# Optimization experiments

Measured on AMD Instinct MI355X. Metric: run time of the kernel, lower is better.

Reference implementation:

```python
import jax, jax.numpy as jnp
import numpy as np

N, F, OUT = 8192, 256, 256


def setup_inputs() -> dict:
    key = jax.random.key(0)
    ks = jax.random.split(key, 8)
    s = 1.0 / np.sqrt(F)
    return {
        "features": jax.random.normal(ks[0], (N, F), jnp.float32),
        "key_features": jax.random.normal(ks[1], (N, F), jnp.float32),
        "adj_matrix": jax.random.uniform(ks[2], (N, N), jnp.float32),
        "W_d": jax.random.normal(ks[3], (2 * F, F), jnp.float32) * (1.0 / np.sqrt(2 * F)),
        "b_d": jnp.zeros((F,), jnp.float32),
        "W_o": jax.random.normal(ks[4], (F, OUT), jnp.float32) * s,
        "b_o": jnp.zeros((OUT,), jnp.float32),
        "W_a": jax.random.normal(ks[5], (F, F), jnp.float32) * s,
        "b_a": jnp.zeros((F,), jnp.float32),
        "W_ao": jax.random.normal(ks[6], (F, OUT), jnp.float32) * s,
        "b_ao": jnp.zeros((OUT,), jnp.float32),
    }


def reference(features, key_features, adj_matrix, W_d, b_d, W_o, b_o, W_a, b_a, W_ao, b_ao):
    n = features.shape[0]
    # masked softmax over rows; self-loop (diagonal) masked out
    neg = jnp.asarray(-1e9, adj_matrix.dtype)
    logits = adj_matrix * 5.0 + jnp.eye(n, dtype=adj_matrix.dtype) * neg
    a = jax.nn.softmax(logits, axis=-1)  # [N, N]
    # sum_j a_ij * concat(x_i, x_j) == concat(x_i * rowsum_i, (A @ X)_i)
    rowsum = jnp.sum(a, axis=-1, keepdims=True)  # == 1, kept for faithfulness
    agg = a @ features  # [N, F]
    neigh = jnp.concatenate([features * rowsum, agg], axis=-1)  # [N, 2F]
    neigh_distill = neigh @ W_d + b_d
    feature_updated = jnp.tanh((features - neigh_distill) @ W_o + b_o)
    # aggregate branch (withAgg=True)
    key_agg = (a @ key_features) @ W_a + b_a
    feature_aggregate = jnp.tanh((key_features + key_agg) @ W_ao + b_ao)
    return (feature_updated, feature_aggregate)
```

## Files before the change

### kernel.cpp

```cpp
#include <hip/hip_runtime.h>
#include <stdint.h>
#include <math.h>


typedef __attribute__((ext_vector_type(4)))  short bf16x4_t;
typedef __attribute__((ext_vector_type(8)))  short bf16x8_t;
typedef __attribute__((ext_vector_type(4)))  float f32x4_t;
typedef __attribute__((ext_vector_type(16))) float f32x16_t;

#define MFMA32(A, B, C) __builtin_amdgcn_mfma_f32_32x32x16_bf16(A, B, C, 0, 0, 0)
#define MFMA16(A, B, C) __builtin_amdgcn_mfma_f32_16x16x32_bf16(A, B, C, 0, 0, 0)

__device__ __forceinline__ unsigned short f2bf(float x) {
    union { float f; unsigned u; } c; c.f = x;
    unsigned u = c.u;
    return (unsigned short)((u + 0x7fffu + ((u >> 16) & 1u)) >> 16);
}
__device__ __forceinline__ unsigned pack2bf(float a, float b) {
    return (unsigned)f2bf(a) | ((unsigned)f2bf(b) << 16);
}
__device__ __forceinline__ float bflo(unsigned u) {
    union { unsigned u; float f; } c; c.u = u << 16; return c.f;
}
__device__ __forceinline__ float bfhi(unsigned u) {
    union { unsigned u; float f; } c; c.u = u & 0xffff0000u; return c.f;
}
__device__ __forceinline__ float exp5(float x) {
    return __builtin_amdgcn_exp2f(7.2134752f * x);
}

__device__ __forceinline__ void gll16(const unsigned short* g, unsigned short* l) {
    __builtin_amdgcn_global_load_lds(
        (const __attribute__((address_space(1))) unsigned int*)(g),
        (__attribute__((address_space(3))) unsigned int*)(l), 16, 0, 0);
}

__global__ __launch_bounds__(256) void transpose_blob(
    const float* __restrict__ src, unsigned short* __restrict__ Xtb,
    unsigned* __restrict__ packdst, int c32base)
{
    __shared__ float tile[32][33];
    const int t = threadIdx.x;
    const int x = t & 31, y4 = (t >> 5) * 4;
    const int r0 = blockIdx.x * 32, c0 = blockIdx.y * 32;
#pragma unroll
    for (int i = 0; i < 4; ++i)
        tile[y4 + i][x] = src[(size_t)(r0 + y4 + i) * 256 + c0 + x];
    __syncthreads();
    const int s = t >> 7, lane = (t >> 1) & 63, e0 = (t & 1) * 4;
    const int kl = s * 16 + (lane >> 5) * 8 + e0;
    const int cl = lane & 31;
    unsigned short* blob = Xtb + ((size_t)blockIdx.x * 16 + (c0 >> 5) + c32base) * 1024;
    uint2 v;
    v.x = pack2bf(tile[kl][cl],     tile[kl + 1][cl]);
    v.y = pack2bf(tile[kl + 2][cl], tile[kl + 3][cl]);
    *(uint2*)(blob + t * 4) = v;
    const int prow = t >> 3, pc = t & 7;
    unsigned* pd = packdst + (size_t)(r0 + prow) * 256 + (c0 >> 1) + pc * 2;
    pd[0] = pack2bf(tile[prow][pc * 4 + 0], tile[prow][pc * 4 + 1]);
    pd[1] = pack2bf(tile[prow][pc * 4 + 2], tile[prow][pc * 4 + 3]);
}

__global__ __launch_bounds__(256) void compose1(
    const float* __restrict__ W_d, const float* __restrict__ W_o,
    const float* __restrict__ b_d, const float* __restrict__ b_o,
    unsigned short* __restrict__ W1t, float* __restrict__ c1)
{
    __shared__ float wrow[256];
    const int k = blockIdx.x, t = threadIdx.x;
    const float* srcrow = (k < 512) ? (W_d + (size_t)k * 256) : b_d;
    wrow[t] = srcrow[t];
    __syncthreads();
    float acc = 0.f;
#pragma unroll 8
    for (int m = 0; m < 256; ++m) acc = fmaf(wrow[m], W_o[(size_t)m * 256 + t], acc);
    if (k < 512)
        W1t[(size_t)t * 512 + k] = f2bf((k < 256 ? W_o[(size_t)k * 256 + t] : 0.f) - acc);
    else
        c1[t] = b_o[t] - acc;
}

__global__ __launch_bounds__(256) void compose2(
    const float* __restrict__ W_a, const float* __restrict__ W_ao,
    const float* __restrict__ b_a, const float* __restrict__ b_ao,
    unsigned short* __restrict__ W2t, float* __restrict__ c2)
{
    __shared__ float wrow[256];
    const int k = blockIdx.x, t = threadIdx.x;
    if (k < 256) {
        W2t[(size_t)t * 512 + k] = f2bf(W_ao[(size_t)k * 256 + t]);
        return;
    }
    const float* srcrow = (k < 512) ? (W_a + (size_t)(k - 256) * 256) : b_a;
    wrow[t] = srcrow[t];
    __syncthreads();
    float acc = 0.f;
#pragma unroll 8
    for (int m = 0; m < 256; ++m) acc = fmaf(wrow[m], W_ao[(size_t)m * 256 + t], acc);
    if (k < 512) W2t[(size_t)t * 512 + k] = f2bf(acc);
    else         c2[t] = b_ao[t] + acc;
}

#define ROWS 32
#define KSLICE 2048
#define NPH 32
#define ASTRIDE 36

struct QA { float4 v[2]; };

__global__ __launch_bounds__(256, 2) void exp_gemm(
    const float* __restrict__ adj, const unsigned short* __restrict__ Xtb,
    unsigned* __restrict__ UpartB, float* __restrict__ sSp)
{
    __shared__ unsigned short sA[2][2][ROWS * ASTRIDE];
    __shared__ unsigned short sB[4][2][4096];

    const int t = threadIdx.x;
    const int w = t >> 6, lane = t & 63, q = lane >> 5, l31 = lane & 31;
    const int xcd = blockIdx.x & 7;
    const int h = xcd >> 1;
    const int rb = ((blockIdx.x >> 3) << 1) | (xcd & 1);
    const int row0 = rb * ROWS;
    const int kbase = h * KSLICE, jbase = h * (KSLICE / 32);

    const int srow = t >> 3, skoff = (t & 7) * 4;
    const int sgrow = row0 + srow;
    const float* adj_row = adj + (size_t)sgrow * 8192 + kbase + skoff;
    const int swoff = srow * ASTRIDE + skoff;

    const unsigned short* XtbW = Xtb + (size_t)jbase * 16384 + (size_t)w * 4096 + lane * 8;
    unsigned short* const sBw = &sB[w][0][0];

    float rs = 0.f;
    f32x16_t acc[4];
#pragma unroll
    for (int ct = 0; ct < 4; ++ct)
#pragma unroll
        for (int e = 0; e < 16; ++e) acc[ct][e] = 0.f;

    QA qa0, qa1, qa2, qa3;

    auto loadAdj = [&](int cidx, QA& qq) {
        qq.v[0] = *(const float4*)(adj_row + (size_t)(cidx * 2 + 0) * 32);
        qq.v[1] = *(const float4*)(adj_row + (size_t)(cidx * 2 + 1) * 32);
    };

    auto stageChunk = [&](int cidx, const QA& qq, int buf) {
#pragma unroll
        for (int ks = 0; ks < 2; ++ks) {
            const float4 v = qq.v[ks];
            float e0 = exp5(v.x);
            float e1 = exp5(v.y);
            float e2 = exp5(v.z);
            float e3 = exp5(v.w);
            const int gk = kbase + (cidx * 2 + ks) * 32 + skoff;
            if (gk + 0 == sgrow) e0 = 0.f;
            if (gk + 1 == sgrow) e1 = 0.f;
            if (gk + 2 == sgrow) e2 = 0.f;
            if (gk + 3 == sgrow) e3 = 0.f;
            rs += (e0 + e1) + (e2 + e3);
            uint2 p; p.x = pack2bf(e0, e1); p.y = pack2bf(e2, e3);
            *(uint2*)(&sA[buf][ks][swoff]) = p;
        }
    };

    auto issueB = [&](int jn, int slot) {
        const unsigned short* src = XtbW + (size_t)jn * 16384;
        unsigned short* dst = sBw + slot * 4096;
#pragma unroll
        for (int k4 = 0; k4 < 8; ++k4)
            gll16(src + k4 * 512, dst + k4 * 512);
    };

    auto consume = [&](int buf, int u, int jnext) {
        const unsigned short* sbp = sBw + u * 4096 + lane * 8;
        bf16x8_t bfr[4][2];
#pragma unroll
        for (int ct = 0; ct < 4; ++ct)
#pragma unroll
            for (int s = 0; s < 2; ++s)
                bfr[ct][s] = *(const bf16x8_t*)(sbp + ct * 1024 + s * 512);
        const unsigned short* sa = &sA[buf][u][0] + l31 * ASTRIDE + q * 8;
        bf16x8_t af[2];
#pragma unroll
        for (int s = 0; s < 2; ++s) {
            const unsigned short* p = sa + s * 16;
            bf16x4_t lo = *(const bf16x4_t*)p;
            bf16x4_t hi = *(const bf16x4_t*)(p + 4);
            af[s] = __builtin_shufflevector(lo, hi, 0, 1, 2, 3, 4, 5, 6, 7);
        }
        asm volatile("s_waitcnt lgkmcnt(0)" ::: "memory");
        issueB(jnext, u);
        __builtin_amdgcn_s_setprio(1);
#pragma unroll
        for (int s = 0; s < 2; ++s)
#pragma unroll
            for (int ct = 0; ct < 4; ++ct)
                acc[ct] = MFMA32(af[s], bfr[ct][s], acc[ct]);
        __builtin_amdgcn_s_setprio(0);
    };

    auto phase = [&](int c, const QA& qstg, QA& qld, int buf) {
        if (c + 1 < NPH) stageChunk(c + 1, qstg, buf ^ 1);
        asm volatile("s_waitcnt vmcnt(10)" ::: "memory");
        consume(buf, 0, (2 * c + 2) & 63);
        asm volatile("s_waitcnt vmcnt(10)" ::: "memory");
        consume(buf, 1, (2 * c + 3) & 63);
        loadAdj((c + 4) & 31, qld);
        asm volatile("s_waitcnt lgkmcnt(0)\n\ts_barrier" ::: "memory");
    };

    issueB(0, 0); issueB(1, 1);
    loadAdj(0, qa0); loadAdj(1, qa1); loadAdj(2, qa2); loadAdj(3, qa3);
    stageChunk(0, qa0, 0);
    asm volatile("s_waitcnt lgkmcnt(0)\n\ts_barrier" ::: "memory");

    for (int c0 = 0; c0 < NPH; c0 += 4) {
        phase(c0 + 0, qa1, qa0, 0);
        phase(c0 + 1, qa2, qa1, 1);
        phase(c0 + 2, qa3, qa2, 0);
        phase(c0 + 3, qa0, qa3, 1);
    }

    rs += __shfl_xor(rs, 1);
    rs += __shfl_xor(rs, 2);
    rs += __shfl_xor(rs, 4);
    if ((t & 7) == 0) sSp[h * 8192 + sgrow] = rs;

    unsigned* upBase = UpartB + (((size_t)h * 256 + rb) * 8 + w * 2) * 1024 + lane;
#pragma unroll
    for (int cp = 0; cp < 2; ++cp)
#pragma unroll
        for (int c2 = 0; c2 < 2; ++c2)
#pragma unroll
            for (int ip = 0; ip < 8; ++ip)
                upBase[(size_t)cp * 1024 + (c2 * 8 + ip) * 64] =
                    pack2bf(acc[cp * 2 + c2][2 * ip], acc[cp * 2 + c2][2 * ip + 1]);
}

__global__ __launch_bounds__(256) void finalize_agg(
    const unsigned* __restrict__ UpartB, const float* __restrict__ sSp,
    unsigned* __restrict__ XcatN, unsigned* __restrict__ Kcat)
{
    __shared__ float sT[32][65];
    __shared__ float sInv[32];

    const int t = threadIdx.x;
    const int rb = blockIdx.x >> 3, wp = blockIdx.x & 7;
    const int row0 = rb * 32;

    if (t < 32) {
        const int r = row0 + t;
        sInv[t] = 1.f / (sSp[r] + sSp[8192 + r] + sSp[16384 + r] + sSp[24576 + r]);
    }

    const int i = t >> 4;
    const int l0 = (t & 15) * 4;
    const int ct2 = i >> 3, ip = i & 7;
    const int qq = l0 >> 5;
    const int rlo = 2 * (ip & 1) + 8 * (ip >> 1) + 4 * qq;
    const int cbase = ct2 * 32 + (l0 & 31);

    float lo[4], hi[4];
#pragma unroll
    for (int j = 0; j < 4; ++j) { lo[j] = 0.f; hi[j] = 0.f; }
#pragma unroll
    for (int h = 0; h < 4; ++h) {
        const unsigned* src = UpartB + (((size_t)h * 256 + rb) * 8 + wp) * 1024
                              + (size_t)i * 64 + l0;
        const uint4 v0 = *(const uint4*)(src);
        const unsigned vv[4] = { v0.x, v0.y, v0.z, v0.w };
#pragma unroll
        for (int j = 0; j < 4; ++j) { lo[j] += bflo(vv[j]); hi[j] += bfhi(vv[j]); }
    }
#pragma unroll
    for (int j = 0; j < 4; ++j) {
        sT[rlo][cbase + j]     = lo[j];
        sT[rlo + 1][cbase + j] = hi[j];
    }
    __syncthreads();

    const int row = t >> 3, cg = (t & 7) * 8;
    const float inv = sInv[row];
    unsigned outv[4];
#pragma unroll
    for (int j = 0; j < 4; ++j)
        outv[j] = pack2bf(sT[row][cg + 2 * j] * inv, sT[row][cg + 2 * j + 1] * inv);
    unsigned* dst = (wp < 4 ? XcatN : Kcat)
                    + (size_t)(row0 + row) * 256 + 128 + (wp & 3) * 32 + (cg >> 1);
    *(uint4*)(dst) = *(const uint4*)(outv);
}

__global__ __launch_bounds__(256) void gemm_out(
    const unsigned short* __restrict__ Aa, const unsigned short* __restrict__ Wta,
    const float* __restrict__ ca,
    const unsigned short* __restrict__ Ab, const unsigned short* __restrict__ Wtb,
    const float* __restrict__ cb,
    float* __restrict__ outa, float* __restrict__ outb)
{
    __shared__ unsigned short sAm[32 * ASTRIDE];
    __shared__ unsigned short sB[256 * ASTRIDE];
    __shared__ float sBias[256];

    const int bid = blockIdx.x;
    const int prob = bid >> 8, tile = bid & 255;
    const unsigned short* A  = prob ? Ab  : Aa;
    const unsigned short* Wt = prob ? Wtb : Wta;
    const float* cvec        = prob ? cb  : ca;
    float* out               = prob ? outb : outa;

    const int t = threadIdx.x, w = t >> 6, lane = t & 63;
    const int m_lo = lane & 15, quad = lane >> 4;
    const int row0 = tile * 32;
    sBias[t] = cvec[t];

    f32x4_t acc[2][4];
#pragma unroll
    for (int a = 0; a < 2; ++a)
#pragma unroll
        for (int b = 0; b < 4; ++b)
#pragma unroll
            for (int e = 0; e < 4; ++e) acc[a][b][e] = 0.f;

    for (int ks = 0; ks < 16; ++ks) {
        const int k0 = ks * 32;
        __syncthreads();
        if (t < 128) {
            bf16x8_t v = *(const bf16x8_t*)(A + (size_t)(row0 + (t >> 2)) * 512 + k0 + (t & 3) * 8);
            unsigned short* d = &sAm[(t >> 2) * ASTRIDE + (t & 3) * 8];
            *(bf16x4_t*)d       = __builtin_shufflevector(v, v, 0, 1, 2, 3);
            *(bf16x4_t*)(d + 4) = __builtin_shufflevector(v, v, 4, 5, 6, 7);
        }
        {
            const unsigned short* src = Wt + (size_t)t * 512 + k0;
            unsigned short* d = &sB[t * ASTRIDE];
#pragma unroll
            for (int j = 0; j < 4; ++j) {
                bf16x8_t v = *(const bf16x8_t*)(src + j * 8);
                *(bf16x4_t*)(d + j * 8)     = __builtin_shufflevector(v, v, 0, 1, 2, 3);
                *(bf16x4_t*)(d + j * 8 + 4) = __builtin_shufflevector(v, v, 4, 5, 6, 7);
            }
        }
        __syncthreads();
        bf16x8_t a0, a1;
        {
            const unsigned short* p = &sAm[m_lo * ASTRIDE + quad * 8];
            bf16x4_t lo = *(const bf16x4_t*)p, hi = *(const bf16x4_t*)(p + 4);
            a0 = __builtin_shufflevector(lo, hi, 0, 1, 2, 3, 4, 5, 6, 7);
            p += 16 * ASTRIDE;
            lo = *(const bf16x4_t*)p; hi = *(const bf16x4_t*)(p + 4);
            a1 = __builtin_shufflevector(lo, hi, 0, 1, 2, 3, 4, 5, 6, 7);
        }
#pragma unroll
        for (int nt = 0; nt < 4; ++nt) {
            const unsigned short* p = &sB[(w * 64 + nt * 16 + m_lo) * ASTRIDE + quad * 8];
            bf16x4_t lo = *(const bf16x4_t*)p, hi = *(const bf16x4_t*)(p + 4);
            bf16x8_t b = __builtin_shufflevector(lo, hi, 0, 1, 2, 3, 4, 5, 6, 7);
            acc[0][nt] = MFMA16(a0, b, acc[0][nt]);
            acc[1][nt] = MFMA16(a1, b, acc[1][nt]);
        }
    }

#pragma unroll
    for (int mt = 0; mt < 2; ++mt)
#pragma unroll
        for (int nt = 0; nt < 4; ++nt) {
            const int col = w * 64 + nt * 16 + m_lo;
#pragma unroll
            for (int r = 0; r < 4; ++r) {
                const int row = row0 + mt * 16 + quad * 4 + r;
                out[(size_t)row * 256 + col] = tanhf(acc[mt][nt][r] + sBias[col]);
            }
        }
}

extern "C" void kernel_launch(void* const* d_in, const int* in_sizes, int n_in,
                              void* d_out, int out_size, void* d_ws, size_t ws_size,
                              hipStream_t stream) {
    const float* features = (const float*)d_in[0];
    const float* key      = (const float*)d_in[1];
    const float* adj      = (const float*)d_in[2];
    const float* W_d  = (const float*)d_in[3];
    const float* b_d  = (const float*)d_in[4];
    const float* W_o  = (const float*)d_in[5];
    const float* b_o  = (const float*)d_in[6];
    const float* W_a  = (const float*)d_in[7];
    const float* b_a  = (const float*)d_in[8];
    const float* W_ao = (const float*)d_in[9];
    const float* b_ao = (const float*)d_in[10];

    float* out1 = (float*)d_out;
    float* out2 = out1 + (size_t)8192 * 256;

    char* ws = (char*)d_ws;
    unsigned short* XcatN = (unsigned short*)(ws);
    unsigned short* Kcat  = (unsigned short*)(ws +  8388608);
    unsigned short* Xtb   = (unsigned short*)(ws + 16777216);
    unsigned*       UpartB= (unsigned*)      (ws + 25165824);
    float*          sSp   = (float*)         (ws + 58720256);
    unsigned short* W1t   = (unsigned short*)(ws + 58851328);
    unsigned short* W2t   = (unsigned short*)(ws + 59113472);
    float*          c1    = (float*)         (ws + 59375616);
    float*          c2    = (float*)         (ws + 59376640);

    dim3 blk(256);
    transpose_blob<<<dim3(256, 8), blk, 0, stream>>>(features, Xtb, (unsigned*)XcatN, 0);
    transpose_blob<<<dim3(256, 8), blk, 0, stream>>>(key, Xtb, (unsigned*)Kcat, 8);
    compose1<<<513, blk, 0, stream>>>(W_d, W_o, b_d, b_o, W1t, c1);
    compose2<<<513, blk, 0, stream>>>(W_a, W_ao, b_a, b_ao, W2t, c2);

    exp_gemm<<<1024, blk, 0, stream>>>(adj, Xtb, UpartB, sSp);
    finalize_agg<<<2048, blk, 0, stream>>>(UpartB, sSp,
                                           (unsigned*)XcatN, (unsigned*)Kcat);

    gemm_out<<<512, blk, 0, stream>>>(XcatN, W1t, c1, Kcat, W2t, c2, out1, out2);
}
```

Baseline: 531.0 us.

## Replace LDS-staged pipelined exp-GEMM with register-direct loads and 512-thread blocks

The exp_gemm kernel drops its shared-memory staging of the exponentiated adjacency and its global_load_lds pipeline for X. Each lane now loads adj directly, computes the exponentials into an MFMA A-fragment in registers, and reads the B fragments straight from global memory. Blocks grow to 512 threads covering 64 rows with a 2x4 wave split, so every wave owns a 32-row by 128-column tile. finalize_agg is re-indexed to match the new partial-sum layout. This removes LDS traffic and barriers but gives up explicit prefetch, and the B tiles are now re-read from global or cache by every row-group wave.

Measured after the change: 636.8 us. +19.9%, slower.

```diff
diff --git a/kernel.cpp b/kernel.cpp
--- a/kernel.cpp
+++ b/kernel.cpp
@@ -27,12 +27,6 @@
 }
 __device__ __forceinline__ float exp5(float x) {
     return __builtin_amdgcn_exp2f(7.2134752f * x);
-}
-
-__device__ __forceinline__ void gll16(const unsigned short* g, unsigned short* l) {
-    __builtin_amdgcn_global_load_lds(
-        (const __attribute__((address_space(1))) unsigned int*)(g),
-        (__attribute__((address_space(3))) unsigned int*)(l), 16, 0, 0);
 }
 
 __global__ __launch_bounds__(256) void transpose_blob(
@@ -101,141 +95,75 @@
     else         c2[t] = b_ao[t] + acc;
 }
 
-#define ROWS 32
-#define KSLICE 2048
-#define NPH 32
 #define ASTRIDE 36
 
-struct QA { float4 v[2]; };
-
-__global__ __launch_bounds__(256, 2) void exp_gemm(
+__global__ __launch_bounds__(512, 3) void exp_gemm(
     const float* __restrict__ adj, const unsigned short* __restrict__ Xtb,
     unsigned* __restrict__ UpartB, float* __restrict__ sSp)
 {
-    __shared__ unsigned short sA[2][2][ROWS * ASTRIDE];
-    __shared__ unsigned short sB[4][2][4096];
-
     const int t = threadIdx.x;
-    const int w = t >> 6, lane = t & 63, q = lane >> 5, l31 = lane & 31;
+    const int w = t >> 6, lane = t & 63, l31 = lane & 31, kh = lane >> 5;
     const int xcd = blockIdx.x & 7;
     const int h = xcd >> 1;
     const int rb = ((blockIdx.x >> 3) << 1) | (xcd & 1);
-    const int row0 = rb * ROWS;
-    const int kbase = h * KSLICE, jbase = h * (KSLICE / 32);
-
-    const int srow = t >> 3, skoff = (t & 7) * 4;
-    const int sgrow = row0 + srow;
-    const float* adj_row = adj + (size_t)sgrow * 8192 + kbase + skoff;
-    const int swoff = srow * ASTRIDE + skoff;
-
-    const unsigned short* XtbW = Xtb + (size_t)jbase * 16384 + (size_t)w * 4096 + lane * 8;
-    unsigned short* const sBw = &sB[w][0][0];
-
+    const int rg = w >> 2, cg = w & 3;
+    const int wrow0 = rb * 64 + rg * 32;
+    const int kbase = h * 2048, jbase = h * 64;
+    const int grow = wrow0 + l31;
+
+    const float* adjp = adj + (size_t)grow * 8192 + kbase + kh * 8;
+    const unsigned short* bbase = Xtb + ((size_t)jbase * 16 + cg * 4) * 1024 + lane * 8;
+
+    f32x16_t acc[4];
+#pragma unroll
+    for (int ct = 0; ct < 4; ++ct)
+#pragma unroll
+        for (int e = 0; e < 16; ++e) acc[ct][e] = 0.f;
     float rs = 0.f;
-    f32x16_t acc[4];
+
+    for (int jj = 0; jj < 64; ++jj) {
+        const float* aj = adjp + jj * 32;
+        const unsigned short* bj = bbase + (size_t)jj * 16384;
+#pragma unroll
+        for (int s = 0; s < 2; ++s) {
+            const float4 a0 = *(const float4*)(aj + s * 16);
+            const float4 a1 = *(const float4*)(aj + s * 16 + 4);
+            float e0 = exp5(a0.x), e1 = exp5(a0.y), e2 = exp5(a0.z), e3 = exp5(a0.w);
+            float e4 = exp5(a1.x), e5 = exp5(a1.y), e6 = exp5(a1.z), e7 = exp5(a1.w);
+            const int kw0 = kbase + jj * 32 + s * 16;
+            if (kw0 + 16 > wrow0 && kw0 < wrow0 + 32) {
+                const int d = grow - (kw0 + kh * 8);
+                if (d == 0) e0 = 0.f;
+                if (d == 1) e1 = 0.f;
+                if (d == 2) e2 = 0.f;
+                if (d == 3) e3 = 0.f;
+                if (d == 4) e4 = 0.f;
+                if (d == 5) e5 = 0.f;
+                if (d == 6) e6 = 0.f;
+                if (d == 7) e7 = 0.f;
+            }
+            rs += ((e0 + e1) + (e2 + e3)) + ((e4 + e5) + (e6 + e7));
+            union { uint4 u; bf16x8_t v; } ca;
+            ca.u.x = pack2bf(e0, e1); ca.u.y = pack2bf(e2, e3);
+            ca.u.z = pack2bf(e4, e5); ca.u.w = pack2bf(e6, e7);
+#pragma unroll
+            for (int ct = 0; ct < 4; ++ct) {
+                const bf16x8_t b = *(const bf16x8_t*)(bj + ct * 1024 + s * 512);
+                acc[ct] = MFMA32(ca.v, b, acc[ct]);
+            }
+        }
+    }
+
+    rs += __shfl_xor(rs, 32);
+    if (cg == 0 && lane < 32) sSp[h * 8192 + wrow0 + lane] = rs;
+
+    unsigned* up = UpartB + ((((size_t)h * 128 + rb) * 2 + rg) * 4 + cg) * 2048 + lane;
 #pragma unroll
     for (int ct = 0; ct < 4; ++ct)
 #pragma unroll
-        for (int e = 0; e < 16; ++e) acc[ct][e] = 0.f;
-
-    QA qa0, qa1, qa2, qa3;
-
-    auto loadAdj = [&](int cidx, QA& qq) {
-        qq.v[0] = *(const float4*)(adj_row + (size_t)(cidx * 2 + 0) * 32);
-        qq.v[1] = *(const float4*)(adj_row + (size_t)(cidx * 2 + 1) * 32);
-    };
-
-    auto stageChunk = [&](int cidx, const QA& qq, int buf) {
-#pragma unroll
-        for (int ks = 0; ks < 2; ++ks) {
-            const float4 v = qq.v[ks];
-            float e0 = exp5(v.x);
-            float e1 = exp5(v.y);
-            float e2 = exp5(v.z);
-            float e3 = exp5(v.w);
-            const int gk = kbase + (cidx * 2 + ks) * 32 + skoff;
-            if (gk + 0 == sgrow) e0 = 0.f;
-            if (gk + 1 == sgrow) e1 = 0.f;
-            if (gk + 2 == sgrow) e2 = 0.f;
-            if (gk + 3 == sgrow) e3 = 0.f;
-            rs += (e0 + e1) + (e2 + e3);
-            uint2 p; p.x = pack2bf(e0, e1); p.y = pack2bf(e2, e3);
-            *(uint2*)(&sA[buf][ks][swoff]) = p;
-        }
-    };
-
-    auto issueB = [&](int jn, int slot) {
-        const unsigned short* src = XtbW + (size_t)jn * 16384;
-        unsigned short* dst = sBw + slot * 4096;
-#pragma unroll
-        for (int k4 = 0; k4 < 8; ++k4)
-            gll16(src + k4 * 512, dst + k4 * 512);
-    };
-
-    auto consume = [&](int buf, int u, int jnext) {
-        const unsigned short* sbp = sBw + u * 4096 + lane * 8;
-        bf16x8_t bfr[4][2];
-#pragma unroll
-        for (int ct = 0; ct < 4; ++ct)
-#pragma unroll
-            for (int s = 0; s < 2; ++s)
-                bfr[ct][s] = *(const bf16x8_t*)(sbp + ct * 1024 + s * 512);
-        const unsigned short* sa = &sA[buf][u][0] + l31 * ASTRIDE + q * 8;
-        bf16x8_t af[2];
-#pragma unroll
-        for (int s = 0; s < 2; ++s) {
-            const unsigned short* p = sa + s * 16;
-            bf16x4_t lo = *(const bf16x4_t*)p;
-            bf16x4_t hi = *(const bf16x4_t*)(p + 4);
-            af[s] = __builtin_shufflevector(lo, hi, 0, 1, 2, 3, 4, 5, 6, 7);
-        }
-        asm volatile("s_waitcnt lgkmcnt(0)" ::: "memory");
-        issueB(jnext, u);
-        __builtin_amdgcn_s_setprio(1);
-#pragma unroll
-        for (int s = 0; s < 2; ++s)
-#pragma unroll
-            for (int ct = 0; ct < 4; ++ct)
-                acc[ct] = MFMA32(af[s], bfr[ct][s], acc[ct]);
-        __builtin_amdgcn_s_setprio(0);
-    };
-
-    auto phase = [&](int c, const QA& qstg, QA& qld, int buf) {
-        if (c + 1 < NPH) stageChunk(c + 1, qstg, buf ^ 1);
-        asm volatile("s_waitcnt vmcnt(10)" ::: "memory");
-        consume(buf, 0, (2 * c + 2) & 63);
-        asm volatile("s_waitcnt vmcnt(10)" ::: "memory");
-        consume(buf, 1, (2 * c + 3) & 63);
-        loadAdj((c + 4) & 31, qld);
-        asm volatile("s_waitcnt lgkmcnt(0)\n\ts_barrier" ::: "memory");
-    };
-
-    issueB(0, 0); issueB(1, 1);
-    loadAdj(0, qa0); loadAdj(1, qa1); loadAdj(2, qa2); loadAdj(3, qa3);
-    stageChunk(0, qa0, 0);
-    asm volatile("s_waitcnt lgkmcnt(0)\n\ts_barrier" ::: "memory");
-
-    for (int c0 = 0; c0 < NPH; c0 += 4) {
-        phase(c0 + 0, qa1, qa0, 0);
-        phase(c0 + 1, qa2, qa1, 1);
-        phase(c0 + 2, qa3, qa2, 0);
-        phase(c0 + 3, qa0, qa3, 1);
-    }
-
-    rs += __shfl_xor(rs, 1);
-    rs += __shfl_xor(rs, 2);
-    rs += __shfl_xor(rs, 4);
-    if ((t & 7) == 0) sSp[h * 8192 + sgrow] = rs;
-
-    unsigned* upBase = UpartB + (((size_t)h * 256 + rb) * 8 + w * 2) * 1024 + lane;
-#pragma unroll
-    for (int cp = 0; cp < 2; ++cp)
-#pragma unroll
-        for (int c2 = 0; c2 < 2; ++c2)
-#pragma unroll
-            for (int ip = 0; ip < 8; ++ip)
-                upBase[(size_t)cp * 1024 + (c2 * 8 + ip) * 64] =
-                    pack2bf(acc[cp * 2 + c2][2 * ip], acc[cp * 2 + c2][2 * ip + 1]);
+        for (int ip = 0; ip < 8; ++ip)
+            up[(size_t)(ct * 8 + ip) * 64] =
+                pack2bf(acc[ct][2 * ip], acc[ct][2 * ip + 1]);
 }
 
 __global__ __launch_bounds__(256) void finalize_agg(
@@ -246,8 +174,9 @@
     __shared__ float sInv[32];
 
     const int t = threadIdx.x;
-    const int rb = blockIdx.x >> 3, wp = blockIdx.x & 7;
-    const int row0 = rb * 32;
+    const int rb32 = blockIdx.x >> 3, g = blockIdx.x & 7;
+    const int rb = rb32 >> 1, rg = rb32 & 1, cg = g >> 1;
+    const int row0 = rb32 * 32;
 
     if (t < 32) {
         const int r = row0 + t;
@@ -256,18 +185,20 @@
 
     const int i = t >> 4;
     const int l0 = (t & 15) * 4;
-    const int ct2 = i >> 3, ip = i & 7;
+    const int ctl = i >> 3, ip = i & 7;
+    const int ct = (g & 1) * 2 + ctl;
     const int qq = l0 >> 5;
     const int rlo = 2 * (ip & 1) + 8 * (ip >> 1) + 4 * qq;
-    const int cbase = ct2 * 32 + (l0 & 31);
+    const int cbase = ctl * 32 + (l0 & 31);
 
     float lo[4], hi[4];
 #pragma unroll
     for (int j = 0; j < 4; ++j) { lo[j] = 0.f; hi[j] = 0.f; }
 #pragma unroll
     for (int h = 0; h < 4; ++h) {
-        const unsigned* src = UpartB + (((size_t)h * 256 + rb) * 8 + wp) * 1024
-                              + (size_t)i * 64 + l0;
+        const unsigned* src = UpartB
+            + ((((size_t)h * 128 + rb) * 2 + rg) * 4 + cg) * 2048
+            + (size_t)(ct * 8 + ip) * 64 + l0;
         const uint4 v0 = *(const uint4*)(src);
         const unsigned vv[4] = { v0.x, v0.y, v0.z, v0.w };
 #pragma unroll
@@ -280,14 +211,14 @@
     }
     __syncthreads();
 
-    const int row = t >> 3, cg = (t & 7) * 8;
+    const int row = t >> 3, c8 = (t & 7) * 8;
     const float inv = sInv[row];
     unsigned outv[4];
 #pragma unroll
     for (int j = 0; j < 4; ++j)
-        outv[j] = pack2bf(sT[row][cg + 2 * j] * inv, sT[row][cg + 2 * j + 1] * inv);
-    unsigned* dst = (wp < 4 ? XcatN : Kcat)
-                    + (size_t)(row0 + row) * 256 + 128 + (wp & 3) * 32 + (cg >> 1);
+        outv[j] = pack2bf(sT[row][c8 + 2 * j] * inv, sT[row][c8 + 2 * j + 1] * inv);
+    unsigned* dst = (g < 4 ? XcatN : Kcat)
+                    + (size_t)(row0 + row) * 256 + 128 + (g & 3) * 32 + (c8 >> 1);
     *(uint4*)(dst) = *(const uint4*)(outv);
 }
 
@@ -409,7 +340,7 @@
     compose1<<<513, blk, 0, stream>>>(W_d, W_o, b_d, b_o, W1t, c1);
     compose2<<<513, blk, 0, stream>>>(W_a, W_ao, b_a, b_ao, W2t, c2);
 
-    exp_gemm<<<1024, blk, 0, stream>>>(adj, Xtb, UpartB, sSp);
+    exp_gemm<<<512, dim3(512), 0, stream>>>(adj, Xtb, UpartB, sSp);
     finalize_agg<<<2048, blk, 0, stream>>>(UpartB, sSp,
                                            (unsigned*)XcatN, (unsigned*)Kcat);
 
```
